# Performance work log

Hardware: AMD Instinct MI355X
Metric: run time of the kernel (lower is better)

## Reference

```python
import jax, jax.numpy as jnp
import numpy as np

N, T, K = 400000, 64, 3


def setup_inputs() -> dict:
    key = jax.random.key(0)
    ks = jax.random.split(key, 6)
    G = jax.random.randint(ks[0], (N, 1), 0, 3).astype(jnp.float32)   # genotype 0/1/2
    S = jax.random.randint(ks[1], (N, T, 1), 0, 2).astype(jnp.float32)  # binary exposure
    C = jax.random.uniform(ks[2], (N, T, 1), dtype=jnp.float32)         # cumulative pack-years (scaled)
    Y = (jax.random.uniform(ks[3], (N, T, 1)) < 0.05).astype(jnp.float32)  # rare binary outcome
    L = jax.random.normal(ks[4], (N, K), dtype=jnp.float32)             # covariates
    kw = jax.random.split(ks[5], 2)
    f32 = jnp.float32
    params = dict(
        psi=jnp.array([0.5], f32),
        gamma_S=jnp.array([0.1], f32),
        gamma_C=jnp.array([0.1], f32),
        gamma_G=jnp.array([0.1], f32),
        gamma_GS=jnp.array([0.0], f32),
        gamma_GC=jnp.array([0.0], f32),
        gamma_L_w=jax.random.normal(kw[0], (1, K), f32) * 0.1,
        log_sigma_Z=jnp.array([-2.0], f32),
        beta_0=jnp.array([-3.0], f32),
        beta_Z=jnp.array([0.5], f32),
        beta_S=jnp.array([0.1], f32),
        beta_G=jnp.array([0.1], f32),
        beta_GS=jnp.array([0.0], f32),
        beta_L_w=jax.random.normal(kw[1], (1, K), f32) * 0.1,
    )
    return dict(G=G, S=S, C=C, Y=Y, L=L, **params)


def reference(G, S, C, Y, L, psi, gamma_S, gamma_C, gamma_G, gamma_GS, gamma_GC,
              gamma_L_w, log_sigma_Z, beta_0, beta_Z, beta_S, beta_G, beta_GS, beta_L_w):
    """Faithful JAX port of HiddenMarkovGFormulaV2.forward_filter (fit_interaction=fit_pack_years=True).
    Returns (Z_filtered (N,T,1), Z_variance (N,T,1), log_likelihood scalar)."""
    sigma2 = jnp.exp(log_sigma_Z) ** 2            # sigma_Z^2, shape (1,)
    gL = L @ gamma_L_w.T                          # (N,1) covariate term for transition
    bL = L @ beta_L_w.T                           # (N,1) covariate term for outcome

    def step(carry, xs):
        Z_mean, Z_var = carry                     # each (N,1)
        S_t, C_t, Y_t = xs                        # each (N,1)
        # hidden state transition
        Z_pred = (psi * Z_mean + gamma_S * S_t + gamma_G * G + gamma_C * C_t
                  + gamma_GS * (G * S_t) + gamma_GC * (G * C_t) + gL)
        Z_pred_var = psi ** 2 * Z_var + sigma2
        # outcome probability
        logit = jnp.clip(beta_0 + beta_Z * Z_pred + beta_S * S_t + beta_G * G
                         + beta_GS * (G * S_t) + bL, -20.0, 20.0)
        p = jax.nn.sigmoid(logit)
        # Laplace-style measurement update
        grad = (Y_t - p) * beta_Z
        hess = beta_Z ** 2 * p * (1.0 - p) + 1e-6
        Z_post_var = 1.0 / (1.0 / Z_pred_var + hess)
        Z_post_mean = Z_pred + Z_post_var * grad
        ll = jnp.sum(Y_t * jnp.log(p + 1e-10) + (1.0 - Y_t) * jnp.log(1.0 - p + 1e-10))
        return (Z_post_mean, Z_post_var), (Z_post_mean, Z_post_var, ll)

    n = G.shape[0]
    Zm0 = jnp.zeros((n, 1), dtype=G.dtype)
    Zv0 = jnp.ones((n, 1), dtype=G.dtype)
    xs = (jnp.swapaxes(S, 0, 1), jnp.swapaxes(C, 0, 1), jnp.swapaxes(Y, 0, 1))  # (T,N,1)
    _, (Zf, Zvf, lls) = jax.lax.scan(step, (Zm0, Zv0), xs)
    Z_filtered = jnp.swapaxes(Zf, 0, 1)   # (N,T,1)
    Z_variance = jnp.swapaxes(Zvf, 0, 1)  # (N,T,1)
    return Z_filtered, Z_variance, jnp.sum(lls)
```

## Files before the change

### kernel.cpp

```cpp
#include <hip/hip_runtime.h>


#define TT 64
#define KK 3
#define NB 256
#define CT 16
#define LDP (NB + 4)

__global__ void zero_ll_kernel(float* ll) { *ll = 0.0f; }

__global__ __launch_bounds__(NB, 4) void hmm_filter_kernel(
    const float* __restrict__ G,
    const float* __restrict__ S,
    const float* __restrict__ C,
    const float* __restrict__ Y,
    const float* __restrict__ L,
    const float* __restrict__ p_psi,
    const float* __restrict__ p_gS,
    const float* __restrict__ p_gC,
    const float* __restrict__ p_gG,
    const float* __restrict__ p_gGS,
    const float* __restrict__ p_gGC,
    const float* __restrict__ p_gLw,
    const float* __restrict__ p_lsZ,
    const float* __restrict__ p_b0,
    const float* __restrict__ p_bZ,
    const float* __restrict__ p_bS,
    const float* __restrict__ p_bG,
    const float* __restrict__ p_bGS,
    const float* __restrict__ p_bLw,
    float* __restrict__ Zf,
    float* __restrict__ Zv,
    float* __restrict__ ll_out,
    int N)
{
    __shared__ float sS [CT][LDP];
    __shared__ float sCY[CT][LDP];
    __shared__ float wave_ll[NB / 64];

    const int tid = threadIdx.x;
    const int n0  = blockIdx.x * NB;
    const int n   = n0 + tid;
    const bool valid = (n < N);

    const float psi  = p_psi[0];
    const float gS   = p_gS[0];
    const float gC   = p_gC[0];
    const float gG   = p_gG[0];
    const float gGS  = p_gGS[0];
    const float gGC  = p_gGC[0];
    const float b0   = p_b0[0];
    const float bZ   = p_bZ[0];
    const float bS   = p_bS[0];
    const float bG   = p_bG[0];
    const float bGS  = p_bGS[0];
    const float esz  = expf(p_lsZ[0]);
    const float sigma2 = esz * esz;
    const float psi2 = psi * psi;
    const float bZ2  = bZ * bZ;
    const float gw0 = p_gLw[0], gw1 = p_gLw[1], gw2 = p_gLw[2];
    const float bw0 = p_bLw[0], bw1 = p_bLw[1], bw2 = p_bLw[2];

    float a_s = 0.0f, a_c = 0.0f, zbase = 0.0f, b_s = 0.0f, lbase = 0.0f;
    if (valid) {
        const float Gv = G[n];
        const float l0 = L[n * KK + 0];
        const float l1 = L[n * KK + 1];
        const float l2 = L[n * KK + 2];
        const float gL = l0 * gw0 + l1 * gw1 + l2 * gw2;
        const float bL = l0 * bw0 + l1 * bw1 + l2 * bw2;
        a_s   = gS + gGS * Gv;
        a_c   = gC + gGC * Gv;
        zbase = gG * Gv + gL;
        b_s   = bS + bGS * Gv;
        lbase = b0 + bG * Gv + bL;
    } else {
        lbase = b0;
    }

    float zm  = 0.0f;
    float zv  = 1.0f;
    float ll2 = 0.0f;

    const float4* S4 = (const float4*)S;
    const float4* C4 = (const float4*)C;
    const float4* Y4 = (const float4*)Y;
    float4* Zf4 = (float4*)Zf;
    float4* Zv4 = (float4*)Zv;

    const int rbase = tid >> 2;
    const int cc    = tid & 3;
    const int tb    = cc * 4;

    float4 rs[4], rc[4], ry[4];

    #pragma unroll
    for (int i = 0; i < 4; ++i) {
        const int nn = n0 + rbase + i * 64;
        if (nn < N) {
            const int gidx = nn * (TT / 4) + cc;
            rs[i] = S4[gidx]; rc[i] = C4[gidx]; ry[i] = Y4[gidx];
        } else {
            rs[i] = make_float4(0, 0, 0, 0);
            rc[i] = rs[i]; ry[i] = rs[i];
        }
    }

    for (int t0 = 0; t0 < TT; t0 += CT) {
        #pragma unroll
        for (int i = 0; i < 4; ++i) {
            const int r = rbase + i * 64;
            sS[tb + 0][r] = rs[i].x; sS[tb + 1][r] = rs[i].y;
            sS[tb + 2][r] = rs[i].z; sS[tb + 3][r] = rs[i].w;
            sCY[tb + 0][r] = __uint_as_float(__float_as_uint(rc[i].x) | (__float_as_uint(ry[i].x) << 8));
            sCY[tb + 1][r] = __uint_as_float(__float_as_uint(rc[i].y) | (__float_as_uint(ry[i].y) << 8));
            sCY[tb + 2][r] = __uint_as_float(__float_as_uint(rc[i].z) | (__float_as_uint(ry[i].z) << 8));
            sCY[tb + 3][r] = __uint_as_float(__float_as_uint(rc[i].w) | (__float_as_uint(ry[i].w) << 8));
        }
        __syncthreads();

        if (t0 + CT < TT) {
            const int fo = ((t0 + CT) >> 2) + cc;
            #pragma unroll
            for (int i = 0; i < 4; ++i) {
                const int nn = n0 + rbase + i * 64;
                if (nn < N) {
                    const int gidx = nn * (TT / 4) + fo;
                    rs[i] = S4[gidx]; rc[i] = C4[gidx]; ry[i] = Y4[gidx];
                }
            }
        }

        #pragma unroll
        for (int t = 0; t < CT; ++t) {
            const float s      = sS[t][tid];
            const unsigned cyb = __float_as_uint(sCY[t][tid]);
            const float c      = __uint_as_float(cyb & 0x7fffffffu);
            const bool  yb     = (cyb >> 31) != 0u;

            const float zpred = fmaf(psi, zm, fmaf(a_s, s, fmaf(a_c, c, zbase)));
            const float zpvar = fmaf(psi2, zv, sigma2);

            float logit = fmaf(bZ, zpred, fmaf(b_s, s, lbase));
            logit = fminf(fmaxf(logit, -20.0f), 20.0f);
            const float p   = __builtin_amdgcn_rcpf(1.0f + __expf(-logit));
            const float omp = 1.0f - p;

            const float ymp = yb ? omp : -p;
            const float sel = yb ? p : omp;

            const float hess = fmaf(bZ2 * p, omp, 1e-6f);
            const float zpostvar  = zpvar * __builtin_amdgcn_rcpf(fmaf(zpvar, hess, 1.0f));
            const float zpostmean = fmaf(zpostvar * bZ, ymp, zpred);

            ll2 += __log2f(sel + 1e-10f);

            zm = zpostmean;
            zv = zpostvar;
            sS [t][tid] = zpostmean;
            sCY[t][tid] = zpostvar;
        }
        __syncthreads();

        #pragma unroll
        for (int i = 0; i < 4; ++i) {
            const int r  = rbase + i * 64;
            const int nn = n0 + r;
            if (nn < N) {
                float4 vf, vv;
                vf.x = sS [tb + 0][r]; vf.y = sS [tb + 1][r];
                vf.z = sS [tb + 2][r]; vf.w = sS [tb + 3][r];
                vv.x = sCY[tb + 0][r]; vv.y = sCY[tb + 1][r];
                vv.z = sCY[tb + 2][r]; vv.w = sCY[tb + 3][r];
                const int gidx = nn * (TT / 4) + (t0 >> 2) + cc;
                Zf4[gidx] = vf;
                Zv4[gidx] = vv;
            }
        }
        __syncthreads();
    }

    float ll = valid ? ll2 * 0.69314718055994531f : 0.0f;
    #pragma unroll
    for (int off = 32; off > 0; off >>= 1) {
        ll += __shfl_down(ll, off, 64);
    }
    const int wid  = tid >> 6;
    const int lane = tid & 63;
    if (lane == 0) wave_ll[wid] = ll;
    __syncthreads();
    if (tid == 0) {
        float sacc = 0.0f;
        #pragma unroll
        for (int w = 0; w < NB / 64; ++w) sacc += wave_ll[w];
        atomicAdd(ll_out, sacc);
    }
}

extern "C" void kernel_launch(void* const* d_in, const int* in_sizes, int n_in,
                              void* d_out, int out_size, void* d_ws, size_t ws_size,
                              hipStream_t stream) {
    const int N = in_sizes[0];

    const float* G   = (const float*)d_in[0];
    const float* S   = (const float*)d_in[1];
    const float* C   = (const float*)d_in[2];
    const float* Y   = (const float*)d_in[3];
    const float* L   = (const float*)d_in[4];
    const float* psi = (const float*)d_in[5];
    const float* gS  = (const float*)d_in[6];
    const float* gC  = (const float*)d_in[7];
    const float* gG  = (const float*)d_in[8];
    const float* gGS = (const float*)d_in[9];
    const float* gGC = (const float*)d_in[10];
    const float* gLw = (const float*)d_in[11];
    const float* lsZ = (const float*)d_in[12];
    const float* b0  = (const float*)d_in[13];
    const float* bZ  = (const float*)d_in[14];
    const float* bS  = (const float*)d_in[15];
    const float* bG  = (const float*)d_in[16];
    const float* bGS = (const float*)d_in[17];
    const float* bLw = (const float*)d_in[18];

    float* out = (float*)d_out;
    float* Zf = out;
    float* Zv = out + (size_t)N * TT;
    float* ll = out + (size_t)2 * N * TT;

    zero_ll_kernel<<<1, 1, 0, stream>>>(ll);

    const int blocks = (N + NB - 1) / NB;
    hmm_filter_kernel<<<blocks, NB, 0, stream>>>(
        G, S, C, Y, L, psi, gS, gC, gG, gGS, gGC, gLw, lsZ,
        b0, bZ, bS, bG, bGS, bLw, Zf, Zv, ll, N);
}
```

Measured before the change: 505.8 us.

## Make LDS staging per-wave, drop block barriers, replace atomic with partial-sum reduce

Each wavefront now stages its own 64 rows of S/C/Y through a private LDS slice, so the transpose needs no __syncthreads and only an lgkmcnt wait. The block shrinks to 128 threads. The cross-block atomicAdd plus zeroing kernel is replaced by per-block partial sums written to workspace and a single-block reduction kernel. This removes barrier stalls between waves and atomic contention, at the cost of relying on wave-level lockstep for LDS correctness and adding a second kernel launch.

```diff
diff --git a/kernel.cpp b/kernel.cpp
--- a/kernel.cpp
+++ b/kernel.cpp
@@ -3,13 +3,26 @@
 
 #define TT 64
 #define KK 3
-#define NB 256
+#define BT 128
+#define WPB (BT / 64)
 #define CT 16
-#define LDP (NB + 4)
-
-__global__ void zero_ll_kernel(float* ll) { *ll = 0.0f; }
-
-__global__ __launch_bounds__(NB, 4) void hmm_filter_kernel(
+#define LDP 66
+
+__global__ __launch_bounds__(256) void ll_reduce_kernel(
+    const float* __restrict__ part, float* __restrict__ ll_out, int nb)
+{
+    float s = 0.0f;
+    for (int i = threadIdx.x; i < nb; i += 256) s += part[i];
+    #pragma unroll
+    for (int off = 32; off > 0; off >>= 1) s += __shfl_down(s, off, 64);
+    __shared__ float ws[4];
+    const int wid = threadIdx.x >> 6, lane = threadIdx.x & 63;
+    if (lane == 0) ws[wid] = s;
+    __syncthreads();
+    if (threadIdx.x == 0) *ll_out = ws[0] + ws[1] + ws[2] + ws[3];
+}
+
+__global__ __launch_bounds__(BT, 4) void hmm_filter_kernel(
     const float* __restrict__ G,
     const float* __restrict__ S,
     const float* __restrict__ C,
@@ -31,16 +44,18 @@
     const float* __restrict__ p_bLw,
     float* __restrict__ Zf,
     float* __restrict__ Zv,
-    float* __restrict__ ll_out,
+    float* __restrict__ ll_part,
     int N)
 {
-    __shared__ float sS [CT][LDP];
-    __shared__ float sCY[CT][LDP];
-    __shared__ float wave_ll[NB / 64];
-
-    const int tid = threadIdx.x;
-    const int n0  = blockIdx.x * NB;
-    const int n   = n0 + tid;
+    __shared__ float sS [WPB][CT][LDP];
+    __shared__ float sCY[WPB][CT][LDP];
+    __shared__ float wll[WPB];
+
+    const int tid   = threadIdx.x;
+    const int w     = tid >> 6;
+    const int l     = tid & 63;
+    const int wbase = blockIdx.x * BT + w * 64;
+    const int n     = wbase + l;
     const bool valid = (n < N);
 
     const float psi  = p_psi[0];
@@ -88,15 +103,15 @@
     float4* Zf4 = (float4*)Zf;
     float4* Zv4 = (float4*)Zv;
 
-    const int rbase = tid >> 2;
-    const int cc    = tid & 3;
-    const int tb    = cc * 4;
+    const int rq = l >> 2;
+    const int cc = l & 3;
+    const int tb = cc * 4;
 
     float4 rs[4], rc[4], ry[4];
 
     #pragma unroll
     for (int i = 0; i < 4; ++i) {
-        const int nn = n0 + rbase + i * 64;
+        const int nn = wbase + rq + i * 16;
         if (nn < N) {
             const int gidx = nn * (TT / 4) + cc;
             rs[i] = S4[gidx]; rc[i] = C4[gidx]; ry[i] = Y4[gidx];
@@ -109,21 +124,20 @@
     for (int t0 = 0; t0 < TT; t0 += CT) {
         #pragma unroll
         for (int i = 0; i < 4; ++i) {
-            const int r = rbase + i * 64;
-            sS[tb + 0][r] = rs[i].x; sS[tb + 1][r] = rs[i].y;
-            sS[tb + 2][r] = rs[i].z; sS[tb + 3][r] = rs[i].w;
-            sCY[tb + 0][r] = __uint_as_float(__float_as_uint(rc[i].x) | (__float_as_uint(ry[i].x) << 8));
-            sCY[tb + 1][r] = __uint_as_float(__float_as_uint(rc[i].y) | (__float_as_uint(ry[i].y) << 8));
-            sCY[tb + 2][r] = __uint_as_float(__float_as_uint(rc[i].z) | (__float_as_uint(ry[i].z) << 8));
-            sCY[tb + 3][r] = __uint_as_float(__float_as_uint(rc[i].w) | (__float_as_uint(ry[i].w) << 8));
-        }
-        __syncthreads();
+            const int r = rq + i * 16;
+            sS[w][tb + 0][r] = rs[i].x; sS[w][tb + 1][r] = rs[i].y;
+            sS[w][tb + 2][r] = rs[i].z; sS[w][tb + 3][r] = rs[i].w;
+            sCY[w][tb + 0][r] = __uint_as_float(__float_as_uint(rc[i].x) | (__float_as_uint(ry[i].x) << 8));
+            sCY[w][tb + 1][r] = __uint_as_float(__float_as_uint(rc[i].y) | (__float_as_uint(ry[i].y) << 8));
+            sCY[w][tb + 2][r] = __uint_as_float(__float_as_uint(rc[i].z) | (__float_as_uint(ry[i].z) << 8));
+            sCY[w][tb + 3][r] = __uint_as_float(__float_as_uint(rc[i].w) | (__float_as_uint(ry[i].w) << 8));
+        }
 
         if (t0 + CT < TT) {
             const int fo = ((t0 + CT) >> 2) + cc;
             #pragma unroll
             for (int i = 0; i < 4; ++i) {
-                const int nn = n0 + rbase + i * 64;
+                const int nn = wbase + rq + i * 16;
                 if (nn < N) {
                     const int gidx = nn * (TT / 4) + fo;
                     rs[i] = S4[gidx]; rc[i] = C4[gidx]; ry[i] = Y4[gidx];
@@ -131,10 +145,12 @@
             }
         }
 
+        asm volatile("s_waitcnt lgkmcnt(0)" ::: "memory");
+
         #pragma unroll
         for (int t = 0; t < CT; ++t) {
-            const float s      = sS[t][tid];
-            const unsigned cyb = __float_as_uint(sCY[t][tid]);
+            const float s      = sS[w][t][l];
+            const unsigned cyb = __float_as_uint(sCY[w][t][l]);
             const float c      = __uint_as_float(cyb & 0x7fffffffu);
             const bool  yb     = (cyb >> 31) != 0u;
 
@@ -157,27 +173,27 @@
 
             zm = zpostmean;
             zv = zpostvar;
-            sS [t][tid] = zpostmean;
-            sCY[t][tid] = zpostvar;
-        }
-        __syncthreads();
+            sS [w][t][l] = zpostmean;
+            sCY[w][t][l] = zpostvar;
+        }
+
+        asm volatile("s_waitcnt lgkmcnt(0)" ::: "memory");
 
         #pragma unroll
         for (int i = 0; i < 4; ++i) {
-            const int r  = rbase + i * 64;
-            const int nn = n0 + r;
+            const int r  = rq + i * 16;
+            const int nn = wbase + r;
             if (nn < N) {
                 float4 vf, vv;
-                vf.x = sS [tb + 0][r]; vf.y = sS [tb + 1][r];
-                vf.z = sS [tb + 2][r]; vf.w = sS [tb + 3][r];
-                vv.x = sCY[tb + 0][r]; vv.y = sCY[tb + 1][r];
-                vv.z = sCY[tb + 2][r]; vv.w = sCY[tb + 3][r];
+                vf.x = sS [w][tb + 0][r]; vf.y = sS [w][tb + 1][r];
+                vf.z = sS [w][tb + 2][r]; vf.w = sS [w][tb + 3][r];
+                vv.x = sCY[w][tb + 0][r]; vv.y = sCY[w][tb + 1][r];
+                vv.z = sCY[w][tb + 2][r]; vv.w = sCY[w][tb + 3][r];
                 const int gidx = nn * (TT / 4) + (t0 >> 2) + cc;
                 Zf4[gidx] = vf;
                 Zv4[gidx] = vv;
             }
         }
-        __syncthreads();
     }
 
     float ll = valid ? ll2 * 0.69314718055994531f : 0.0f;
@@ -185,15 +201,13 @@
     for (int off = 32; off > 0; off >>= 1) {
         ll += __shfl_down(ll, off, 64);
     }
-    const int wid  = tid >> 6;
-    const int lane = tid & 63;
-    if (lane == 0) wave_ll[wid] = ll;
+    if (l == 0) wll[w] = ll;
     __syncthreads();
     if (tid == 0) {
         float sacc = 0.0f;
         #pragma unroll
-        for (int w = 0; w < NB / 64; ++w) sacc += wave_ll[w];
-        atomicAdd(ll_out, sacc);
+        for (int ww = 0; ww < WPB; ++ww) sacc += wll[ww];
+        ll_part[blockIdx.x] = sacc;
     }
 }
 
@@ -227,10 +241,11 @@
     float* Zv = out + (size_t)N * TT;
     float* ll = out + (size_t)2 * N * TT;
 
-    zero_ll_kernel<<<1, 1, 0, stream>>>(ll);
-
-    const int blocks = (N + NB - 1) / NB;
-    hmm_filter_kernel<<<blocks, NB, 0, stream>>>(
+    float* ll_part = (float*)d_ws;
+
+    const int blocks = (N + BT - 1) / BT;
+    hmm_filter_kernel<<<blocks, BT, 0, stream>>>(
         G, S, C, Y, L, psi, gS, gC, gG, gGS, gGC, gLw, lsZ,
-        b0, bZ, bS, bG, bGS, bLw, Zf, Zv, ll, N);
+        b0, bZ, bS, bG, bGS, bLw, Zf, Zv, ll_part, N);
+    ll_reduce_kernel<<<1, 256, 0, stream>>>(ll_part, ll, blocks);
 }
```

Result: no change. 505.3 us (-0.1%).
